# Performance work log

Hardware: AMD Instinct MI355X
Metric: run time of the kernel (lower is better)

Reference implementation:

```python
import jax, jax.numpy as jnp
import numpy as np

EPS = 1e-6

def _rmsnorm(x, gamma):
    rms = jax.lax.rsqrt(jnp.mean(x * x, axis=-1, keepdims=True) + EPS)
    return x * rms * gamma

def _rotate_half(x):
    d = x.shape[-1] // 2
    return jnp.concatenate((-x[..., d:], x[..., :d]), axis=-1)

def setup_inputs() -> dict:
    key = jax.random.key(0)
    ks = jax.random.split(key, 6)
    B, S, H, NH = 2, 4096, 1024, 16
    hd = H // NH
    hidden_states = jax.random.normal(ks[0], (B, S, H), dtype=jnp.float32)
    rope_cos = jax.random.uniform(ks[1], (1, S, hd), dtype=jnp.float32)
    rope_sin = jax.random.uniform(ks[2], (1, S, hd), dtype=jnp.float32)
    W_qkv = jax.random.normal(ks[3], (H, 3 * H), dtype=jnp.float32) * (H ** -0.5)
    W_o = jax.random.normal(ks[4], (H, H), dtype=jnp.float32) * (H ** -0.5)
    gamma_q = jnp.ones((hd,), dtype=jnp.float32)
    gamma_k = jnp.ones((hd,), dtype=jnp.float32)
    return {"hidden_states": hidden_states, "rope_cos": rope_cos, "rope_sin": rope_sin,
            "W_qkv": W_qkv, "W_o": W_o, "gamma_q": gamma_q, "gamma_k": gamma_k}

def reference(hidden_states, rope_cos, rope_sin, W_qkv, W_o, gamma_q, gamma_k):
    B, S, H = hidden_states.shape
    NH = 16
    hd = H // NH
    qkv = hidden_states @ W_qkv  # [B,S,3H]
    q, k, v = jnp.split(qkv, 3, axis=-1)
    def to_heads(x):
        return x.reshape(B, S, NH, hd).transpose(0, 2, 1, 3)  # [B,NH,S,hd]
    q, k, v = to_heads(q), to_heads(k), to_heads(v)
    q = _rmsnorm(q, gamma_q)
    k = _rmsnorm(k, gamma_k)
    cos = rope_cos[:, None, :, :]  # [1,1,S,hd]
    sin = rope_sin[:, None, :, :]
    q = q * cos + _rotate_half(q) * sin
    k = k * cos + _rotate_half(k) * sin
    scores = jnp.einsum('bhqd,bhkd->bhqk', q, k) / (hd ** 0.5)
    causal = jnp.tril(jnp.ones((S, S), dtype=bool))
    scores = jnp.where(causal, scores, -jnp.inf)
    attn = jax.nn.softmax(scores, axis=-1)
    out = jnp.einsum('bhqk,bhkd->bhqd', attn, v)
    out = out.transpose(0, 2, 1, 3).reshape(B, S, H)
    return out @ W_o
```

## Files before the change

### kernel.cpp

```cpp
#include <hip/hip_runtime.h>
#include <stdint.h>

typedef unsigned short u16;
typedef __attribute__((ext_vector_type(8))) u16   u16x8;
typedef __attribute__((ext_vector_type(4))) u16   u16x4;
typedef __attribute__((ext_vector_type(8))) __bf16 bf16x8;
typedef __attribute__((ext_vector_type(4))) float  f32x4;

__device__ __forceinline__ u16 f2bf(float f) {
  union { float f; unsigned u; } x; x.f = f;
  unsigned r = x.u + 0x7fffu + ((x.u >> 16) & 1u);
  return (u16)(r >> 16);
}
__device__ __forceinline__ float bf2f(u16 h) {
  union { unsigned u; float f; } x; x.u = ((unsigned)h) << 16;
  return x.f;
}
__device__ __forceinline__ float fexp2(float x) {
#if __has_builtin(__builtin_amdgcn_exp2f)
  return __builtin_amdgcn_exp2f(x);
#else
  return __expf(x * 0.69314718055994531f);
#endif
}
__device__ __forceinline__ void gload_lds16(const void* g, void* l) {
  __builtin_amdgcn_global_load_lds(
      (__attribute__((address_space(1))) void*)(void*)g,
      (__attribute__((address_space(3))) void*)l, 16, 0, 0);
}
__device__ __forceinline__ bf16x8 ldfrag(const u16* p) {
  return __builtin_bit_cast(bf16x8, *(const u16x8*)p);
}
#define MFMA_BF16(a, b, c) __builtin_amdgcn_mfma_f32_16x16x32_bf16(a, b, c, 0, 0, 0)

__global__ __launch_bounds__(256) void k_f32_to_bf16(const float* __restrict__ in,
                                                     u16* __restrict__ out, int n) {
  int i = (blockIdx.x * 256 + threadIdx.x) * 4;
  if (i >= n) return;
  float4 v = *(const float4*)(in + i);
  u16x4 o; o.x = f2bf(v.x); o.y = f2bf(v.y); o.z = f2bf(v.z); o.w = f2bf(v.w);
  *(u16x4*)(out + i) = o;
}

__global__ __launch_bounds__(256) void k_transpose_bf16(const float* __restrict__ in,
                                                        u16* __restrict__ out,
                                                        int R, int C) {
  __shared__ float tile[32][33];
  int c0 = blockIdx.x * 32, r0 = blockIdx.y * 32;
  int tx = threadIdx.x, ty = threadIdx.y;
#pragma unroll
  for (int i = 0; i < 32; i += 8)
    tile[ty + i][tx] = in[(size_t)(r0 + ty + i) * C + c0 + tx];
  __syncthreads();
#pragma unroll
  for (int i = 0; i < 32; i += 8)
    out[(size_t)(c0 + ty + i) * R + r0 + tx] = f2bf(tile[tx][ty + i]);
}

__global__ __launch_bounds__(256) void k_gemm_qkv(const u16* __restrict__ A,
                                                  const u16* __restrict__ Bt,
                                                  u16* __restrict__ Q,
                                                  u16* __restrict__ Kb,
                                                  u16* __restrict__ Vt) {
  const int K = 1024;
  __shared__ u16 As[128 * 32];
  __shared__ u16 Bs[128 * 32];
  int tid = threadIdx.x;
  int wave = tid >> 6, lane = tid & 63, quad = lane >> 4, l15 = lane & 15;
  int m0 = blockIdx.y * 128, n0 = blockIdx.x * 128;
  int wm = (wave >> 1) * 64, wn = (wave & 1) * 64;
  f32x4 acc[4][4] = {};
  const u16* Ag = A + (size_t)m0 * K;
  const u16* Bg = Bt + (size_t)n0 * K;
  int lr = lane >> 2, lk = (lane & 3) * 8;

  for (int k0 = 0; k0 < K; k0 += 32) {
    __syncthreads();
#pragma unroll
    for (int i = 0; i < 2; i++) {
      int c = wave * 2 + i;
      gload_lds16(Ag + (size_t)(c * 16 + lr) * K + k0 + lk, &As[c * 512]);
      gload_lds16(Bg + (size_t)(c * 16 + lr) * K + k0 + lk, &Bs[c * 512]);
    }
    __syncthreads();
    bf16x8 af[4], bf[4];
#pragma unroll
    for (int mi = 0; mi < 4; mi++) af[mi] = ldfrag(&As[(wm + mi * 16 + l15) * 32 + quad * 8]);
#pragma unroll
    for (int ni = 0; ni < 4; ni++) bf[ni] = ldfrag(&Bs[(wn + ni * 16 + l15) * 32 + quad * 8]);
#pragma unroll
    for (int mi = 0; mi < 4; mi++)
#pragma unroll
      for (int ni = 0; ni < 4; ni++)
        acc[mi][ni] = MFMA_BF16(af[mi], bf[ni], acc[mi][ni]);
  }
  int sec = n0 >> 10;
#pragma unroll
  for (int mi = 0; mi < 4; mi++) {
    int rowb = m0 + wm + mi * 16 + quad * 4;
#pragma unroll
    for (int ni = 0; ni < 4; ni++) {
      int col = n0 + wn + ni * 16 + l15;
      int cc = col & 1023, h = cc >> 6, d = cc & 63;
#pragma unroll
      for (int r = 0; r < 4; r++) {
        int rg = rowb + r, b = rg >> 12, s = rg & 4095;
        u16 v = f2bf(acc[mi][ni][r]);
        size_t bh = (size_t)(b * 16 + h);
        if (sec == 0)      Q [(bh * 4096 + s) * 64 + d] = v;
        else if (sec == 1) Kb[(bh * 4096 + s) * 64 + d] = v;
        else               Vt[(bh * 64 + d) * 4096 + s] = v;
      }
    }
  }
}

__global__ __launch_bounds__(256) void k_rms_rope(u16* __restrict__ buf,
                                                  const float* __restrict__ gamma,
                                                  const float* __restrict__ cosb,
                                                  const float* __restrict__ sinb,
                                                  float scale) {
  int rid = blockIdx.x * 16 + (threadIdx.x >> 4);
  int l = threadIdx.x & 15;
  int s = rid & 4095;
  int d0 = l * 4;
  size_t idx = (size_t)rid * 64 + d0;
  u16x4 xv = *(const u16x4*)(buf + idx);
  float x0 = bf2f(xv.x), x1 = bf2f(xv.y), x2 = bf2f(xv.z), x3 = bf2f(xv.w);
  float ss = x0 * x0 + x1 * x1 + x2 * x2 + x3 * x3;
#pragma unroll
  for (int off = 1; off < 16; off <<= 1) ss += __shfl_xor(ss, off);
  float rms = rsqrtf(ss * (1.0f / 64.0f) + 1e-6f);
  float4 g = *(const float4*)(gamma + d0);
  float n0 = x0 * rms * g.x, n1 = x1 * rms * g.y, n2 = x2 * rms * g.z, n3 = x3 * rms * g.w;
  float p0 = __shfl_xor(n0, 8), p1 = __shfl_xor(n1, 8);
  float p2 = __shfl_xor(n2, 8), p3 = __shfl_xor(n3, 8);
  float sgn = (l < 8) ? -1.f : 1.f;
  float4 c = *(const float4*)(cosb + s * 64 + d0);
  float4 sn = *(const float4*)(sinb + s * 64 + d0);
  u16x4 o;
  o.x = f2bf((n0 * c.x + sgn * p0 * sn.x) * scale);
  o.y = f2bf((n1 * c.y + sgn * p1 * sn.y) * scale);
  o.z = f2bf((n2 * c.z + sgn * p2 * sn.z) * scale);
  o.w = f2bf((n3 * c.w + sgn * p3 * sn.w) * scale);
  *(u16x4*)(buf + idx) = o;
}

__device__ __forceinline__ void stage_k(const u16* Kg0, int kj, u16* Kbuf,
                                        int wave, int klr, int klc) {
  const u16* Kg = Kg0 + (size_t)kj * 128 * 64;
#pragma unroll
  for (int i = 0; i < 2; i++) {
    int c = wave * 2 + i;
    gload_lds16(Kg + (size_t)(c * 8 + klr) * 64 + (klc ^ klr) * 8, Kbuf + c * 512);
  }
}
__device__ __forceinline__ void stage_v(const u16* Vg0, int kj, u16* Vbuf,
                                        int wave, int quad, int l15) {
  const u16* Vg = Vg0 + kj * 128;
#pragma unroll
  for (int i = 0; i < 2; i++) {
    int c = wave * 2 + i;
    int vr = c * 4 + quad;
    gload_lds16(Vg + (size_t)vr * 4096 + (l15 ^ (vr & 15)) * 8, Vbuf + c * 512);
  }
}

__global__ __launch_bounds__(512, 4) void k_attn(const u16* __restrict__ Qb,
                                                 const u16* __restrict__ Kg_all,
                                                 const u16* __restrict__ Vtb,
                                                 u16* __restrict__ Ob) {
  __shared__ u16 Ks[2][128 * 64];
  __shared__ u16 Vts[64 * 128];
  __shared__ u16 Ps[8][16 * 40];
  const int PSTR = 40;
  int t = blockIdx.x, bhi = blockIdx.y;
  int tid = threadIdx.x, wave = tid >> 6, lane = tid & 63, quad = lane >> 4, l15 = lane & 15;
  const u16* Kg0 = Kg_all + (size_t)bhi * 4096 * 64;
  const u16* Vg0 = Vtb + (size_t)bhi * 64 * 4096;
  u16* Pw = Ps[wave];
  int klr = lane >> 3, klc = lane & 7;
  int b = bhi >> 4, h = bhi & 15;

  u16x8 ou;
#pragma unroll
  for (int i = 0; i < 8; i++) ou[i] = 0x3F80;
  bf16x8 ones = __builtin_bit_cast(bf16x8, ou);
  const f32x4 minit = {-47.f, -47.f, -47.f, -47.f};

#pragma unroll 1
  for (int tt = 0; tt < 2; tt++) {
    int qi = (tt == 0) ? (31 - t) : t;
    const u16* Qg = Qb + ((size_t)bhi * 4096 + qi * 128) * 64;
    bf16x8 aq[2];
#pragma unroll
    for (int ks = 0; ks < 2; ks++)
      aq[ks] = ldfrag(Qg + (size_t)(wave * 16 + l15) * 64 + ks * 32 + quad * 8);
    f32x4 oacc[4] = {};
    f32x4 lacc = {};

    if (tt) __syncthreads();
    stage_k(Kg0, 0, Ks[0], wave, klr, klc);

#pragma unroll 1
    for (int kj = 0; kj <= qi; kj++) {
      int cur = kj & 1;
      __syncthreads();
      if (kj < qi) stage_k(Kg0, kj + 1, Ks[cur ^ 1], wave, klr, klc);
      stage_v(Vg0, kj, Vts, wave, quad, l15);
      f32x4 sa[8];
#pragma unroll
      for (int nb = 0; nb < 8; nb++) sa[nb] = minit;
      __builtin_amdgcn_s_setprio(1);
#pragma unroll
      for (int ks = 0; ks < 2; ks++) {
#pragma unroll
        for (int nb = 0; nb < 8; nb++) {
          bf16x8 bk = ldfrag(&Ks[cur][(nb * 16 + l15) * 64 + (((ks * 4 + quad) ^ (l15 & 7)) << 3)]);
          sa[nb] = MFMA_BF16(aq[ks], bk, sa[nb]);
        }
      }
      __builtin_amdgcn_s_setprio(0);
      if (kj == qi) {
#pragma unroll
        for (int nb = 0; nb < 8; nb++)
#pragma unroll
          for (int r = 0; r < 4; r++) {
            int rowi = wave * 16 + quad * 4 + r;
            int coli = nb * 16 + l15;
            if (coli > rowi) sa[nb][r] = -1e30f;
          }
      }
#pragma unroll
      for (int nb = 0; nb < 8; nb++)
#pragma unroll
        for (int r = 0; r < 4; r++)
          sa[nb][r] = fexp2(sa[nb][r]);
      __syncthreads();
#pragma unroll
      for (int ks = 0; ks < 4; ks++) {
#pragma unroll
        for (int r = 0; r < 4; r++) {
          int prow = quad * 4 + r;
          Pw[prow * PSTR + l15]      = f2bf(sa[2 * ks][r]);
          Pw[prow * PSTR + 16 + l15] = f2bf(sa[2 * ks + 1][r]);
        }
        bf16x8 ap = ldfrag(&Pw[l15 * PSTR + quad * 8]);
        __builtin_amdgcn_s_setprio(1);
#pragma unroll
        for (int oni = 0; oni < 4; oni++) {
          bf16x8 bv = ldfrag(&Vts[(oni * 16 + l15) * 128 + (((ks * 4 + quad) ^ l15) << 3)]);
          oacc[oni] = MFMA_BF16(ap, bv, oacc[oni]);
        }
        lacc = MFMA_BF16(ap, ones, lacc);
        __builtin_amdgcn_s_setprio(0);
      }
    }
#pragma unroll
    for (int oni = 0; oni < 4; oni++)
#pragma unroll
      for (int r = 0; r < 4; r++) {
        float v = oacc[oni][r] / lacc[r];
        int srow = qi * 128 + wave * 16 + quad * 4 + r;
        int d = oni * 16 + l15;
        Ob[((size_t)(b * 4096 + srow)) * 1024 + h * 64 + d] = f2bf(v);
      }
  }
}

__global__ __launch_bounds__(256) void k_gemm_out(const u16* __restrict__ A,
                                                  const u16* __restrict__ Bt,
                                                  float* __restrict__ C) {
  const int K = 1024, N = 1024;
  __shared__ u16 As[128 * 32];
  __shared__ u16 Bs[128 * 32];
  int tid = threadIdx.x;
  int wave = tid >> 6, lane = tid & 63, quad = lane >> 4, l15 = lane & 15;
  int m0 = blockIdx.y * 128, n0 = blockIdx.x * 128;
  int wm = (wave >> 1) * 64, wn = (wave & 1) * 64;
  f32x4 acc[4][4] = {};
  const u16* Ag = A + (size_t)m0 * K;
  const u16* Bg = Bt + (size_t)n0 * K;
  int lr = lane >> 2, lk = (lane & 3) * 8;

  for (int k0 = 0; k0 < K; k0 += 32) {
    __syncthreads();
#pragma unroll
    for (int i = 0; i < 2; i++) {
      int c = wave * 2 + i;
      gload_lds16(Ag + (size_t)(c * 16 + lr) * K + k0 + lk, &As[c * 512]);
      gload_lds16(Bg + (size_t)(c * 16 + lr) * K + k0 + lk, &Bs[c * 512]);
    }
    __syncthreads();
    bf16x8 af[4], bf[4];
#pragma unroll
    for (int mi = 0; mi < 4; mi++) af[mi] = ldfrag(&As[(wm + mi * 16 + l15) * 32 + quad * 8]);
#pragma unroll
    for (int ni = 0; ni < 4; ni++) bf[ni] = ldfrag(&Bs[(wn + ni * 16 + l15) * 32 + quad * 8]);
#pragma unroll
    for (int mi = 0; mi < 4; mi++)
#pragma unroll
      for (int ni = 0; ni < 4; ni++)
        acc[mi][ni] = MFMA_BF16(af[mi], bf[ni], acc[mi][ni]);
  }
#pragma unroll
  for (int mi = 0; mi < 4; mi++) {
    int rowb = m0 + wm + mi * 16 + quad * 4;
#pragma unroll
    for (int ni = 0; ni < 4; ni++) {
      int col = n0 + wn + ni * 16 + l15;
#pragma unroll
      for (int r = 0; r < 4; r++)
        C[(size_t)(rowb + r) * N + col] = acc[mi][ni][r];
    }
  }
}

extern "C" void kernel_launch(void* const* d_in, const int* in_sizes, int n_in,
                              void* d_out, int out_size, void* d_ws, size_t ws_size,
                              hipStream_t stream) {
  (void)in_sizes; (void)n_in; (void)out_size; (void)ws_size;
  const float* hs   = (const float*)d_in[0];
  const float* cosb = (const float*)d_in[1];
  const float* sinb = (const float*)d_in[2];
  const float* wqkv = (const float*)d_in[3];
  const float* wo   = (const float*)d_in[4];
  const float* gq   = (const float*)d_in[5];
  const float* gk   = (const float*)d_in[6];
  float* out = (float*)d_out;

  char* ws = (char*)d_ws;
  u16* Xb    = (u16*)(ws);
  u16* Wqkvt = (u16*)(ws + 16777216);
  u16* Wot   = (u16*)(ws + 23068672);
  u16* Qb    = (u16*)(ws + 25165824);
  u16* Kb    = (u16*)(ws + 41943040);
  u16* Vtb   = (u16*)(ws + 58720256);
  u16* Ab    = (u16*)(ws + 75497472);

  k_f32_to_bf16<<<8192, 256, 0, stream>>>(hs, Xb, 8388608);
  k_transpose_bf16<<<dim3(96, 32), dim3(32, 8), 0, stream>>>(wqkv, Wqkvt, 1024, 3072);
  k_transpose_bf16<<<dim3(32, 32), dim3(32, 8), 0, stream>>>(wo, Wot, 1024, 1024);
  k_gemm_qkv<<<dim3(24, 64), 256, 0, stream>>>(Xb, Wqkvt, Qb, Kb, Vtb);
  k_rms_rope<<<8192, 256, 0, stream>>>(Qb, gq, cosb, sinb, 0.18033688011112042f);
  k_rms_rope<<<8192, 256, 0, stream>>>(Kb, gk, cosb, sinb, 1.0f);
  k_attn<<<dim3(16, 32), 512, 0, stream>>>(Qb, Kb, Vtb, Ab);
  k_gemm_out<<<dim3(8, 64), 256, 0, stream>>>(Ab, Wot, out);
}
```

Baseline: 350.8 us.

## Double query rows per attention block to reuse staged K/V tiles

Each attention block now processes one 256-row query tile, with each wave handling two 16-row fragments, instead of two paired 128-row tiles. Every K fragment read from LDS feeds two QK MFMAs, and every V fragment feeds two PV MFMAs. This halves shared-memory and global K/V traffic per unit of work. Load balance no longer comes from pairing tiles; it comes from reversing the tile order for half of the heads. The cost is more live registers (two score and accumulator sets) under the 512x4 launch bound, which risks spilling, plus uneven per-block work.

```diff
diff --git a/kernel.cpp b/kernel.cpp
--- a/kernel.cpp
+++ b/kernel.cpp
@@ -172,9 +172,10 @@
                                                  u16* __restrict__ Ob) {
   __shared__ u16 Ks[2][128 * 64];
   __shared__ u16 Vts[64 * 128];
-  __shared__ u16 Ps[8][16 * 40];
+  __shared__ u16 Ps[8][32 * 40];
   const int PSTR = 40;
-  int t = blockIdx.x, bhi = blockIdx.y;
+  int bhi = blockIdx.y;
+  int qi = (bhi < 16) ? blockIdx.x : (15 - blockIdx.x);
   int tid = threadIdx.x, wave = tid >> 6, lane = tid & 63, quad = lane >> 4, l15 = lane & 15;
   const u16* Kg0 = Kg_all + (size_t)bhi * 4096 * 64;
   const u16* Vg0 = Vtb + (size_t)bhi * 64 * 4096;
@@ -188,84 +189,98 @@
   bf16x8 ones = __builtin_bit_cast(bf16x8, ou);
   const f32x4 minit = {-47.f, -47.f, -47.f, -47.f};
 
+  const u16* Qg = Qb + ((size_t)bhi * 4096 + qi * 256) * 64;
+  bf16x8 aq[2][2];
+#pragma unroll
+  for (int mi = 0; mi < 2; mi++)
+#pragma unroll
+    for (int ks = 0; ks < 2; ks++)
+      aq[mi][ks] = ldfrag(Qg + (size_t)(wave * 32 + mi * 16 + l15) * 64 + ks * 32 + quad * 8);
+  f32x4 oacc[2][4] = {};
+  f32x4 lacc[2] = {};
+
+  stage_k(Kg0, 0, Ks[0], wave, klr, klc);
+  int kjmax = 2 * qi + 1;
+
 #pragma unroll 1
-  for (int tt = 0; tt < 2; tt++) {
-    int qi = (tt == 0) ? (31 - t) : t;
-    const u16* Qg = Qb + ((size_t)bhi * 4096 + qi * 128) * 64;
-    bf16x8 aq[2];
-#pragma unroll
-    for (int ks = 0; ks < 2; ks++)
-      aq[ks] = ldfrag(Qg + (size_t)(wave * 16 + l15) * 64 + ks * 32 + quad * 8);
-    f32x4 oacc[4] = {};
-    f32x4 lacc = {};
-
-    if (tt) __syncthreads();
-    stage_k(Kg0, 0, Ks[0], wave, klr, klc);
-
-#pragma unroll 1
-    for (int kj = 0; kj <= qi; kj++) {
-      int cur = kj & 1;
-      __syncthreads();
-      if (kj < qi) stage_k(Kg0, kj + 1, Ks[cur ^ 1], wave, klr, klc);
-      stage_v(Vg0, kj, Vts, wave, quad, l15);
-      f32x4 sa[8];
-#pragma unroll
-      for (int nb = 0; nb < 8; nb++) sa[nb] = minit;
+  for (int kj = 0; kj <= kjmax; kj++) {
+    int cur = kj & 1;
+    __syncthreads();
+    if (kj < kjmax) stage_k(Kg0, kj + 1, Ks[cur ^ 1], wave, klr, klc);
+    stage_v(Vg0, kj, Vts, wave, quad, l15);
+    f32x4 sa[2][8];
+#pragma unroll
+    for (int mi = 0; mi < 2; mi++)
+#pragma unroll
+      for (int nb = 0; nb < 8; nb++) sa[mi][nb] = minit;
+    __builtin_amdgcn_s_setprio(1);
+#pragma unroll
+    for (int ks = 0; ks < 2; ks++) {
+#pragma unroll
+      for (int nb = 0; nb < 8; nb++) {
+        bf16x8 bk = ldfrag(&Ks[cur][(nb * 16 + l15) * 64 + (((ks * 4 + quad) ^ (l15 & 7)) << 3)]);
+        sa[0][nb] = MFMA_BF16(aq[0][ks], bk, sa[0][nb]);
+        sa[1][nb] = MFMA_BF16(aq[1][ks], bk, sa[1][nb]);
+      }
+    }
+    __builtin_amdgcn_s_setprio(0);
+    if (kj >= 2 * qi) {
+      int d128 = (kj - 2 * qi) * 128;
+#pragma unroll
+      for (int mi = 0; mi < 2; mi++)
+#pragma unroll
+        for (int nb = 0; nb < 8; nb++)
+#pragma unroll
+          for (int r = 0; r < 4; r++) {
+            int rowi = wave * 32 + mi * 16 + quad * 4 + r;
+            int coli = nb * 16 + l15;
+            if (coli > rowi - d128) sa[mi][nb][r] = -1e30f;
+          }
+    }
+#pragma unroll
+    for (int mi = 0; mi < 2; mi++)
+#pragma unroll
+      for (int nb = 0; nb < 8; nb++)
+#pragma unroll
+        for (int r = 0; r < 4; r++)
+          sa[mi][nb][r] = fexp2(sa[mi][nb][r]);
+    __syncthreads();
+#pragma unroll
+    for (int ks = 0; ks < 4; ks++) {
+      bf16x8 ap[2];
+#pragma unroll
+      for (int mi = 0; mi < 2; mi++) {
+#pragma unroll
+        for (int r = 0; r < 4; r++) {
+          int prow = mi * 16 + quad * 4 + r;
+          Pw[prow * PSTR + l15]      = f2bf(sa[mi][2 * ks][r]);
+          Pw[prow * PSTR + 16 + l15] = f2bf(sa[mi][2 * ks + 1][r]);
+        }
+        ap[mi] = ldfrag(&Pw[(mi * 16 + l15) * PSTR + quad * 8]);
+      }
       __builtin_amdgcn_s_setprio(1);
 #pragma unroll
-      for (int ks = 0; ks < 2; ks++) {
-#pragma unroll
-        for (int nb = 0; nb < 8; nb++) {
-          bf16x8 bk = ldfrag(&Ks[cur][(nb * 16 + l15) * 64 + (((ks * 4 + quad) ^ (l15 & 7)) << 3)]);
-          sa[nb] = MFMA_BF16(aq[ks], bk, sa[nb]);
-        }
-      }
+      for (int oni = 0; oni < 4; oni++) {
+        bf16x8 bv = ldfrag(&Vts[(oni * 16 + l15) * 128 + (((ks * 4 + quad) ^ l15) << 3)]);
+        oacc[0][oni] = MFMA_BF16(ap[0], bv, oacc[0][oni]);
+        oacc[1][oni] = MFMA_BF16(ap[1], bv, oacc[1][oni]);
+      }
+      lacc[0] = MFMA_BF16(ap[0], ones, lacc[0]);
+      lacc[1] = MFMA_BF16(ap[1], ones, lacc[1]);
       __builtin_amdgcn_s_setprio(0);
-      if (kj == qi) {
-#pragma unroll
-        for (int nb = 0; nb < 8; nb++)
-#pragma unroll
-          for (int r = 0; r < 4; r++) {
-            int rowi = wave * 16 + quad * 4 + r;
-            int coli = nb * 16 + l15;
-            if (coli > rowi) sa[nb][r] = -1e30f;
-          }
-      }
-#pragma unroll
-      for (int nb = 0; nb < 8; nb++)
-#pragma unroll
-        for (int r = 0; r < 4; r++)
-          sa[nb][r] = fexp2(sa[nb][r]);
-      __syncthreads();
-#pragma unroll
-      for (int ks = 0; ks < 4; ks++) {
-#pragma unroll
-        for (int r = 0; r < 4; r++) {
-          int prow = quad * 4 + r;
-          Pw[prow * PSTR + l15]      = f2bf(sa[2 * ks][r]);
-          Pw[prow * PSTR + 16 + l15] = f2bf(sa[2 * ks + 1][r]);
-        }
-        bf16x8 ap = ldfrag(&Pw[l15 * PSTR + quad * 8]);
-        __builtin_amdgcn_s_setprio(1);
-#pragma unroll
-        for (int oni = 0; oni < 4; oni++) {
-          bf16x8 bv = ldfrag(&Vts[(oni * 16 + l15) * 128 + (((ks * 4 + quad) ^ l15) << 3)]);
-          oacc[oni] = MFMA_BF16(ap, bv, oacc[oni]);
-        }
-        lacc = MFMA_BF16(ap, ones, lacc);
-        __builtin_amdgcn_s_setprio(0);
-      }
-    }
+    }
+  }
+#pragma unroll
+  for (int mi = 0; mi < 2; mi++)
 #pragma unroll
     for (int oni = 0; oni < 4; oni++)
 #pragma unroll
       for (int r = 0; r < 4; r++) {
-        float v = oacc[oni][r] / lacc[r];
-        int srow = qi * 128 + wave * 16 + quad * 4 + r;
+        float v = oacc[mi][oni][r] / lacc[mi][r];
+        int srow = qi * 256 + wave * 32 + mi * 16 + quad * 4 + r;
         int d = oni * 16 + l15;
         Ob[((size_t)(b * 4096 + srow)) * 1024 + h * 64 + d] = f2bf(v);
       }
-  }
 }
 
 __global__ __launch_bounds__(256) void k_gemm_out(const u16* __restrict__ A,
```

Result: slower. 514.8 us (+46.7%).
